# Performance work log

Measured on AMD Instinct MI355X. Metric: run time of the kernel, lower is better.

The kernel has to match this reference:

```python
import jax, jax.numpy as jnp
import numpy as np

N = 50000
E = 800000
IN_DIM = 256
HID = 32
HEADS = 4
OUT_DIM = 40
NEG_SLOPE = 0.2


def gat_layer(x, src, dst, W, a_src, a_dst, b, n_nodes, heads, ch, concat):
    # x: [N, F_in], W: [F_in, heads*ch], a_src/a_dst: [heads, ch], b: [out]
    h = (x @ W).reshape(n_nodes, heads, ch)                 # [N,H,C]
    alpha_s = jnp.einsum('nhc,hc->nh', h, a_src)            # [N,H]
    alpha_d = jnp.einsum('nhc,hc->nh', h, a_dst)            # [N,H]
    e = jax.nn.leaky_relu(alpha_s[src] + alpha_d[dst], NEG_SLOPE)  # [E,H]
    # segment softmax over destination neighborhoods (self-loops guarantee nonempty)
    m = jax.ops.segment_max(e, dst, num_segments=n_nodes)   # [N,H]
    e = jnp.exp(e - m[dst])
    denom = jax.ops.segment_sum(e, dst, num_segments=n_nodes)
    alpha = e / (denom[dst] + 1e-16)                         # [E,H]
    msg = h[src] * alpha[:, :, None]                         # [E,H,C]
    out = jax.ops.segment_sum(msg, dst, num_segments=n_nodes)  # [N,H,C]
    out = out.reshape(n_nodes, heads * ch) if concat else out.mean(axis=1)
    return out + b


def setup_inputs() -> dict:
    key = jax.random.key(0)
    ks = jax.random.split(key, 10)
    x = jax.random.normal(ks[0], (N, IN_DIM), dtype=jnp.float32)
    edge_index = jax.random.randint(ks[1], (2, E), 0, N, dtype=jnp.int32)
    s1 = 1.0 / np.sqrt(IN_DIM)
    s2 = 1.0 / np.sqrt(HID * HEADS)
    return {
        'x': x,
        'edge_index': edge_index,
        'W1': jax.random.normal(ks[2], (IN_DIM, HEADS * HID), dtype=jnp.float32) * s1,
        'a_src1': jax.random.normal(ks[3], (HEADS, HID), dtype=jnp.float32) * s1,
        'a_dst1': jax.random.normal(ks[4], (HEADS, HID), dtype=jnp.float32) * s1,
        'b1': jnp.zeros((HEADS * HID,), dtype=jnp.float32),
        'W2': jax.random.normal(ks[5], (HEADS * HID, OUT_DIM), dtype=jnp.float32) * s2,
        'a_src2': jax.random.normal(ks[6], (1, OUT_DIM), dtype=jnp.float32) * s2,
        'a_dst2': jax.random.normal(ks[7], (1, OUT_DIM), dtype=jnp.float32) * s2,
        'b2': jnp.zeros((OUT_DIM,), dtype=jnp.float32),
    }


def reference(x, edge_index, W1, a_src1, a_dst1, b1, W2, a_src2, a_dst2, b2):
    # PyG GATConv adds self-loops by default
    loops = jnp.arange(N, dtype=edge_index.dtype)
    src = jnp.concatenate([edge_index[0], loops])
    dst = jnp.concatenate([edge_index[1], loops])
    h = gat_layer(x, src, dst, W1, a_src1, a_dst1, b1, N, HEADS, HID, True)
    h = jax.nn.relu(h)
    out = gat_layer(h, src, dst, W2, a_src2, a_dst2, b2, N, 1, OUT_DIM, False)
    return jax.nn.log_softmax(out, axis=1)
```

## Files before the change

### kernel.cpp

```cpp
#include <hip/hip_runtime.h>
#include <math.h>

#define N_NODES 50000
#define N_EDGES 800000
#define IN_DIM  256
#define F1      128
#define HEADS   4
#define OUT_DIM 40
#define NEG     0.2f

#define NB   391
#define CAP  3072
#define EB   4096
#define PREW 16
#define G1B  782

#define DCAP 96

typedef __attribute__((ext_vector_type(8))) short short8;
typedef __attribute__((ext_vector_type(4))) float float4v;

__device__ __forceinline__ unsigned short f2bf(float f) {
  unsigned int u = __float_as_uint(f);
  u += 0x7FFF + ((u >> 16) & 1);
  return (unsigned short)(u >> 16);
}
__device__ __forceinline__ float bf2f(unsigned short h) {
  return __uint_as_float((unsigned int)h << 16);
}
__device__ __forceinline__ float bflo(unsigned int u) { return __uint_as_float(u << 16); }
__device__ __forceinline__ float bfhi(unsigned int u) { return __uint_as_float(u & 0xffff0000u); }

__device__ __forceinline__ float lrelu(float e) { return e > 0.f ? e : e * NEG; }

__device__ __forceinline__ void gload_lds16(const void* g, void* l) {
  __builtin_amdgcn_global_load_lds(
      (const __attribute__((address_space(1))) unsigned int*)g,
      (__attribute__((address_space(3))) unsigned int*)l, 16, 0, 0);
}

__global__ __launch_bounds__(256) void pre_kernel(const float* __restrict__ W1,
                                                  unsigned short* __restrict__ wHi,
                                                  unsigned short* __restrict__ wLo,
                                                  const int* __restrict__ ei,
                                                  int* __restrict__ gcnt,
                                                  int2* __restrict__ gbucket) {
  __shared__ int smem[EB * 2 + NB * 3];
  if (blockIdx.x < PREW) {
    int tid = blockIdx.x * 256 + threadIdx.x;
    int kk = tid >> 9;
    int rest = tid & 511;
    int t = rest >> 6;
    int lane = rest & 63;
    int q = lane >> 4;
    int ln = lane & 15;
    int n = t * 16 + ln;
    unsigned int hi[4], lo[4];
#pragma unroll
    for (int jj = 0; jj < 4; jj++) {
      unsigned short h0, h1, l0, l1;
      {
        float v = W1[(kk * 32 + q * 8 + jj * 2) * F1 + n];
        h0 = f2bf(v); l0 = f2bf(v - bf2f(h0));
      }
      {
        float v = W1[(kk * 32 + q * 8 + jj * 2 + 1) * F1 + n];
        h1 = f2bf(v); l1 = f2bf(v - bf2f(h1));
      }
      hi[jj] = (unsigned int)h0 | ((unsigned int)h1 << 16);
      lo[jj] = (unsigned int)l0 | ((unsigned int)l1 << 16);
    }
    size_t base = (size_t)tid * 8;
    *(uint4*)&wHi[base] = make_uint4(hi[0], hi[1], hi[2], hi[3]);
    *(uint4*)&wLo[base] = make_uint4(lo[0], lo[1], lo[2], lo[3]);
  } else {
    int* ls = smem;
    int* ld = smem + EB;
    int* lcnt = smem + 2 * EB;
    int* lcur = lcnt + NB;
    int* gbaseS = lcur + NB;
    int tid = threadIdx.x;
    size_t base = (size_t)(blockIdx.x - PREW) * EB;
    for (int t = tid; t < NB; t += 256) { lcnt[t] = 0; lcur[t] = 0; }
    __syncthreads();
#pragma unroll
    for (int l = 0; l < EB / 256; l++) {
      int li = l * 256 + tid;
      size_t idx = base + li;
      int s = 0, d = -1;
      if (idx < N_EDGES) {
        s = ei[idx];
        d = ei[N_EDGES + idx];
        atomicAdd(&lcnt[d >> 7], 1);
      }
      ls[li] = s;
      ld[li] = d;
    }
    __syncthreads();
    for (int t = tid; t < NB; t += 256) gbaseS[t] = atomicAdd(&gcnt[t], lcnt[t]);
    __syncthreads();
#pragma unroll
    for (int l = 0; l < EB / 256; l++) {
      int li = l * 256 + tid;
      int d = ld[li];
      if (d >= 0) {
        int b = d >> 7;
        int r = gbaseS[b] + atomicAdd(&lcur[b], 1);
        if (r >= CAP) r = CAP - 1;
        gbucket[(size_t)b * CAP + r] = make_int2(ls[li], d);
      }
    }
  }
}

__global__ __launch_bounds__(256) void mid_kernel(
    const float* __restrict__ x, const unsigned short* __restrict__ wHi,
    const unsigned short* __restrict__ wLo,
    const float* __restrict__ a_src, const float* __restrict__ a_dst,
    unsigned short* __restrict__ h1b, float* __restrict__ as1, float* __restrict__ ad1,
    const int2* __restrict__ gbucket, const int* __restrict__ gcnt,
    int* __restrict__ row_ptr, int* __restrict__ col) {
  __shared__ short8 smem[2048];
  if (blockIdx.x < G1B) {
    short8 (*Bsh)[1024] = (short8(*)[1024])smem;
    int bid = blockIdx.x;
    int tid = threadIdx.x;
    int w = tid >> 6;
    int lane = tid & 63;
    int q = lane >> 4;
    int ln = lane & 15;
    int rowBase = bid * 64 + w * 16;
    int rowA = rowBase + ln;
    int rowAc = rowA < N_NODES ? rowA : N_NODES - 1;
    float4v acc[8];
#pragma unroll
    for (int t = 0; t < 8; t++) acc[t] = (float4v){0.f, 0.f, 0.f, 0.f};
    const short8* bhp = (const short8*)wHi;
    const short8* blp = (const short8*)wLo;

    auto prefetch = [&](int kk, int buf) {
#pragma unroll
      for (int c = 0; c < 2; c++) {
        int chunk = w * 2 + c;
        gload_lds16(bhp + (size_t)kk * 512 + chunk * 64 + lane, &Bsh[buf][chunk * 64]);
        gload_lds16(blp + (size_t)kk * 512 + chunk * 64 + lane, &Bsh[buf][512 + chunk * 64]);
      }
    };

    const float4* xbase = (const float4*)(x + (size_t)rowAc * IN_DIM + q * 8);
    float4 a0 = xbase[0];
    float4 a1 = xbase[1];
    prefetch(0, 0);
    __syncthreads();

#pragma unroll 1
    for (int kk = 0; kk < 8; kk++) {
      int buf = kk & 1;
      if (kk < 7) prefetch(kk + 1, buf ^ 1);
      int kn = (kk < 7) ? kk + 1 : 7;
      float4 n0 = xbase[kn * 8];
      float4 n1 = xbase[kn * 8 + 1];
      float av[8] = {a0.x, a0.y, a0.z, a0.w, a1.x, a1.y, a1.z, a1.w};
      short8 ahi, alo;
#pragma unroll
      for (int j = 0; j < 8; j++) {
        unsigned short hh = f2bf(av[j]);
        ahi[j] = (short)hh;
        alo[j] = (short)f2bf(av[j] - bf2f(hh));
      }
      const short8* bs = &Bsh[buf][0];
#pragma unroll
      for (int t = 0; t < 8; t++) {
        short8 bh = bs[t * 64 + lane];
        short8 bl = bs[512 + t * 64 + lane];
        acc[t] = __builtin_amdgcn_mfma_f32_16x16x32_bf16(ahi, bh, acc[t], 0, 0, 0);
        acc[t] = __builtin_amdgcn_mfma_f32_16x16x32_bf16(ahi, bl, acc[t], 0, 0, 0);
        acc[t] = __builtin_amdgcn_mfma_f32_16x16x32_bf16(alo, bh, acc[t], 0, 0, 0);
      }
      a0 = n0;
      a1 = n1;
      if (kk < 7) __syncthreads();
    }

    float asv[8], adv[8];
#pragma unroll
    for (int t = 0; t < 8; t++) {
      asv[t] = a_src[t * 16 + ln];
      adv[t] = a_dst[t * 16 + ln];
    }
#pragma unroll
    for (int reg = 0; reg < 4; reg++) {
      int r = rowBase + q * 4 + reg;
      bool valid = (r < N_NODES);
      if (valid) {
#pragma unroll
        for (int t = 0; t < 8; t++)
          h1b[(size_t)r * F1 + t * 16 + ln] = f2bf(acc[t][reg]);
      }
#pragma unroll
      for (int h = 0; h < 4; h++) {
        float sa = acc[2 * h][reg] * asv[2 * h] + acc[2 * h + 1][reg] * asv[2 * h + 1];
        float sd = acc[2 * h][reg] * adv[2 * h] + acc[2 * h + 1][reg] * adv[2 * h + 1];
#pragma unroll
        for (int off = 1; off < 16; off <<= 1) {
          sa += __shfl_xor(sa, off);
          sd += __shfl_xor(sd, off);
        }
        if (ln == 0 && valid) {
          as1[r * 4 + h] = sa;
          ad1[r * 4 + h] = sd;
        }
      }
    }
  } else {
    int2* ent = (int2*)smem;
    int* hcnt = (int*)(ent + CAP);
    int* sc   = hcnt + 128;
    int* cur  = sc + 128;
    int* red  = cur + 128;
    int b = blockIdx.x - G1B;
    int tid = threadIdx.x;
    int cnt = gcnt[b]; if (cnt > CAP) cnt = CAP;
    if (tid < 128) hcnt[tid] = 0;
    int part = 0;
    for (int i = tid; i < b; i += 256) part += gcnt[i];
#pragma unroll
    for (int off = 32; off > 0; off >>= 1) part += __shfl_xor(part, off);
    if ((tid & 63) == 0) red[tid >> 6] = part;
    __syncthreads();
    int base = red[0] + red[1] + red[2] + red[3];
    for (int i = tid; i < cnt; i += 256) {
      int2 e = gbucket[(size_t)b * CAP + i];
      ent[i] = e;
      atomicAdd(&hcnt[e.y & 127], 1);
    }
    __syncthreads();
    if (tid < 128) sc[tid] = hcnt[tid];
    __syncthreads();
    for (int off = 1; off < 128; off <<= 1) {
      int t = 0;
      if (tid < 128 && tid >= off) t = sc[tid - off];
      __syncthreads();
      if (tid < 128) sc[tid] += t;
      __syncthreads();
    }
    if (tid < 128) {
      int excl = sc[tid] - hcnt[tid];
      cur[tid] = excl;
      int node = (b << 7) + tid;
      if (node < N_NODES) row_ptr[node] = base + excl;
    }
    if (b == 0 && tid == 0) row_ptr[N_NODES] = N_EDGES;
    __syncthreads();
    for (int i = tid; i < cnt; i += 256) {
      int2 e = ent[i];
      int r = atomicAdd(&cur[e.y & 127], 1);
      col[base + r] = e.x;
    }
  }
}

__global__ __launch_bounds__(256) void gather1_kernel(
    const unsigned short* __restrict__ h1b, const float* __restrict__ as1,
    const float* __restrict__ ad1, const float* __restrict__ b1,
    const int* __restrict__ row_ptr, const int* __restrict__ col,
    float* __restrict__ x2) {
  __shared__ float4 wsh[4][DCAP];
  __shared__ int ssh[4][DCAP];
  int wv = threadIdx.x >> 6;
  int n = blockIdx.x * 4 + wv;
  if (n >= N_NODES) return;
  int lane = threadIdx.x & 63;
  int start = row_ptr[n];
  int deg = row_ptr[n + 1] - start;
  bool fast = (deg + 1) <= DCAP;
  float4 ad = *(const float4*)&ad1[n * 4];
  float s0 = 0.f, s1 = 0.f, s2 = 0.f, s3 = 0.f;
  for (int i = lane; i <= deg; i += 64) {
    int src = (i < deg) ? col[start + i] : n;
    float4 as = *(const float4*)&as1[src * 4];
    float e0 = __expf(lrelu(as.x + ad.x));
    float e1 = __expf(lrelu(as.y + ad.y));
    float e2 = __expf(lrelu(as.z + ad.z));
    float e3 = __expf(lrelu(as.w + ad.w));
    s0 += e0; s1 += e1; s2 += e2; s3 += e3;
    if (fast) {
      ssh[wv][i] = src;
      wsh[wv][i] = make_float4(e0, e1, e2, e3);
    }
  }
#pragma unroll
  for (int off = 32; off > 0; off >>= 1) {
    s0 += __shfl_xor(s0, off);
    s1 += __shfl_xor(s1, off);
    s2 += __shfl_xor(s2, off);
    s3 += __shfl_xor(s3, off);
  }
  int slot = lane >> 4;
  int lane16 = lane & 15;
  int head = lane16 >> 2;
  float rsh = (head == 0) ? s0 : (head == 1) ? s1 : (head == 2) ? s2 : s3;
  rsh = 1.f / (rsh + 1e-16f);
  float4 accA = make_float4(0.f, 0.f, 0.f, 0.f);
  float4 accB = make_float4(0.f, 0.f, 0.f, 0.f);
  if (fast) {
    const float* wp = (const float*)&wsh[wv][0];
    int i = slot;
    for (; i + 4 <= deg; i += 8) {
      int sA = ssh[wv][i];
      int sB = ssh[wv][i + 4];
      float wA = wp[i * 4 + head] * rsh;
      float wB = wp[(i + 4) * 4 + head] * rsh;
      uint4 uA = *(const uint4*)(h1b + (size_t)sA * F1 + lane16 * 8);
      uint4 uB = *(const uint4*)(h1b + (size_t)sB * F1 + lane16 * 8);
      accA.x += wA * bflo(uA.x); accA.y += wA * bfhi(uA.x);
      accA.z += wA * bflo(uA.y); accA.w += wA * bfhi(uA.y);
      accB.x += wA * bflo(uA.z); accB.y += wA * bfhi(uA.z);
      accB.z += wA * bflo(uA.w); accB.w += wA * bfhi(uA.w);
      accA.x += wB * bflo(uB.x); accA.y += wB * bfhi(uB.x);
      accA.z += wB * bflo(uB.y); accA.w += wB * bfhi(uB.y);
      accB.x += wB * bflo(uB.z); accB.y += wB * bfhi(uB.z);
      accB.z += wB * bflo(uB.w); accB.w += wB * bfhi(uB.w);
    }
    if (i <= deg) {
      int s = ssh[wv][i];
      float w = wp[i * 4 + head] * rsh;
      uint4 u = *(const uint4*)(h1b + (size_t)s * F1 + lane16 * 8);
      accA.x += w * bflo(u.x); accA.y += w * bfhi(u.x);
      accA.z += w * bflo(u.y); accA.w += w * bfhi(u.y);
      accB.x += w * bflo(u.z); accB.y += w * bfhi(u.z);
      accB.z += w * bflo(u.w); accB.w += w * bfhi(u.w);
    }
  } else {
    float adh = (head == 0) ? ad.x : (head == 1) ? ad.y : (head == 2) ? ad.z : ad.w;
    for (int i = slot; i <= deg; i += 4) {
      int src = (i < deg) ? col[start + i] : n;
      float w = __expf(lrelu(as1[src * 4 + head] + adh)) * rsh;
      uint4 u = *(const uint4*)(h1b + (size_t)src * F1 + lane16 * 8);
      accA.x += w * bflo(u.x); accA.y += w * bfhi(u.x);
      accA.z += w * bflo(u.y); accA.w += w * bfhi(u.y);
      accB.x += w * bflo(u.z); accB.y += w * bfhi(u.z);
      accB.z += w * bflo(u.w); accB.w += w * bfhi(u.w);
    }
  }
#pragma unroll
  for (int off = 16; off <= 32; off <<= 1) {
    accA.x += __shfl_xor(accA.x, off); accA.y += __shfl_xor(accA.y, off);
    accA.z += __shfl_xor(accA.z, off); accA.w += __shfl_xor(accA.w, off);
    accB.x += __shfl_xor(accB.x, off); accB.y += __shfl_xor(accB.y, off);
    accB.z += __shfl_xor(accB.z, off); accB.w += __shfl_xor(accB.w, off);
  }
  if (slot == 0) {
    float4 bA = *(const float4*)&b1[lane16 * 8];
    float4 bB = *(const float4*)&b1[lane16 * 8 + 4];
    float4 oA, oB;
    oA.x = fmaxf(accA.x + bA.x, 0.f); oA.y = fmaxf(accA.y + bA.y, 0.f);
    oA.z = fmaxf(accA.z + bA.z, 0.f); oA.w = fmaxf(accA.w + bA.w, 0.f);
    oB.x = fmaxf(accB.x + bB.x, 0.f); oB.y = fmaxf(accB.y + bB.y, 0.f);
    oB.z = fmaxf(accB.z + bB.z, 0.f); oB.w = fmaxf(accB.w + bB.w, 0.f);
    *(float4*)&x2[(size_t)n * F1 + lane16 * 8] = oA;
    *(float4*)&x2[(size_t)n * F1 + lane16 * 8 + 4] = oB;
  }
}

__global__ __launch_bounds__(256) void gemm2_kernel(
    const float* __restrict__ x2, const float* __restrict__ W2,
    const float* __restrict__ asv, const float* __restrict__ adv,
    unsigned short* __restrict__ h2b, float* __restrict__ as2, float* __restrict__ ad2) {
  __shared__ float xs[64][132];
  __shared__ float W2s[128][44];
  __shared__ float asv_s[40], adv_s[40];
  int tid = threadIdx.x;
  int bm = blockIdx.x * 64;
#pragma unroll
  for (int l = 0; l < 8; l++) {
    int idx = tid + l * 256;
    int r = idx >> 5;
    int c4 = (idx & 31) << 2;
    float4 v = make_float4(0.f, 0.f, 0.f, 0.f);
    if (bm + r < N_NODES) v = *(const float4*)&x2[(size_t)(bm + r) * F1 + c4];
    *(float4*)&xs[r][c4] = v;
  }
#pragma unroll
  for (int l = 0; l < 5; l++) {
    int idx = tid + l * 256;
    int k = idx / 10;
    int c4 = (idx - k * 10) * 4;
    *(float4*)&W2s[k][c4] = *(const float4*)&W2[k * OUT_DIM + c4];
  }
  if (tid < OUT_DIM) { asv_s[tid] = asv[tid]; adv_s[tid] = adv[tid]; }
  __syncthreads();
  int r = tid >> 2;
  int cb = (tid & 3) * 10;
  float acc[10] = {0.f};
  for (int k = 0; k < F1; k++) {
    float xv = xs[r][k];
#pragma unroll
    for (int c = 0; c < 10; c++) acc[c] += xv * W2s[k][cb + c];
  }
  int grow = bm + r;
  float sa = 0.f, sd = 0.f;
#pragma unroll
  for (int c = 0; c < 10; c++) {
    sa += acc[c] * asv_s[cb + c];
    sd += acc[c] * adv_s[cb + c];
  }
#pragma unroll
  for (int off = 1; off < 4; off <<= 1) {
    sa += __shfl_xor(sa, off);
    sd += __shfl_xor(sd, off);
  }
  if (grow < N_NODES) {
#pragma unroll
    for (int c = 0; c < 10; c += 2) {
      unsigned int p = ((unsigned int)f2bf(acc[c + 1]) << 16) | f2bf(acc[c]);
      *(unsigned int*)&h2b[(size_t)grow * OUT_DIM + cb + c] = p;
    }
    if ((tid & 3) == 0) { as2[grow] = sa; ad2[grow] = sd; }
  }
}

__global__ __launch_bounds__(256) void gather2_kernel(
    const unsigned short* __restrict__ h2b, const float* __restrict__ as2,
    const float* __restrict__ ad2, const float* __restrict__ b2,
    const int* __restrict__ row_ptr, const int* __restrict__ col,
    float* __restrict__ out) {
  __shared__ float w2sh[4][DCAP];
  __shared__ int s2sh[4][DCAP];
  int wv = threadIdx.x >> 6;
  int n = blockIdx.x * 4 + wv;
  if (n >= N_NODES) return;
  int lane = threadIdx.x & 63;
  int start = row_ptr[n];
  int deg = row_ptr[n + 1] - start;
  bool fast = (deg + 1) <= DCAP;
  float adh = ad2[n];
  float part = 0.f;
  for (int i = lane; i <= deg; i += 64) {
    int src = (i < deg) ? col[start + i] : n;
    float e = __expf(lrelu(as2[src] + adh));
    part += e;
    if (fast) { s2sh[wv][i] = src; w2sh[wv][i] = e; }
  }
#pragma unroll
  for (int off = 32; off > 0; off >>= 1) part += __shfl_xor(part, off);
  float rs = 1.f / (part + 1e-16f);
  int slot = lane / 5;
  int c = lane - slot * 5;
  float4 accA = make_float4(0.f, 0.f, 0.f, 0.f);
  float4 accB = make_float4(0.f, 0.f, 0.f, 0.f);
  if (slot < 12) {
    if (fast) {
      for (int i = slot; i <= deg; i += 12) {
        int src = s2sh[wv][i];
        float wgt = w2sh[wv][i] * rs;
        uint4 u = *(const uint4*)(h2b + (size_t)src * OUT_DIM + c * 8);
        accA.x += wgt * bflo(u.x); accA.y += wgt * bfhi(u.x);
        accA.z += wgt * bflo(u.y); accA.w += wgt * bfhi(u.y);
        accB.x += wgt * bflo(u.z); accB.y += wgt * bfhi(u.z);
        accB.z += wgt * bflo(u.w); accB.w += wgt * bfhi(u.w);
      }
    } else {
      for (int i = slot; i <= deg; i += 12) {
        int src = (i < deg) ? col[start + i] : n;
        float wgt = __expf(lrelu(as2[src] + adh)) * rs;
        uint4 u = *(const uint4*)(h2b + (size_t)src * OUT_DIM + c * 8);
        accA.x += wgt * bflo(u.x); accA.y += wgt * bfhi(u.x);
        accA.z += wgt * bflo(u.y); accA.w += wgt * bfhi(u.y);
        accB.x += wgt * bflo(u.z); accB.y += wgt * bfhi(u.z);
        accB.z += wgt * bflo(u.w); accB.w += wgt * bfhi(u.w);
      }
    }
  }
  {
    float v[8] = {accA.x, accA.y, accA.z, accA.w, accB.x, accB.y, accB.z, accB.w};
#pragma unroll
    for (int k = 0; k < 8; k++) v[k] += __shfl(v[k], lane + 30);
#pragma unroll
    for (int k = 0; k < 8; k++) v[k] += __shfl(v[k], lane + 15);
    float t1[8], t2[8];
#pragma unroll
    for (int k = 0; k < 8; k++) t1[k] = __shfl(v[k], lane + 5);
#pragma unroll
    for (int k = 0; k < 8; k++) t2[k] = __shfl(v[k], lane + 10);
#pragma unroll
    for (int k = 0; k < 8; k++) v[k] += t1[k] + t2[k];
    accA.x = v[0]; accA.y = v[1]; accA.z = v[2]; accA.w = v[3];
    accB.x = v[4]; accB.y = v[5]; accB.z = v[6]; accB.w = v[7];
  }
  bool owner = (slot == 0);
  float vals[8] = {accA.x, accA.y, accA.z, accA.w, accB.x, accB.y, accB.z, accB.w};
  float lmax = -1e30f, lsum = 0.f;
  if (owner) {
#pragma unroll
    for (int k = 0; k < 8; k++) {
      vals[k] += b2[c * 8 + k];
      lmax = fmaxf(lmax, vals[k]);
    }
  }
  float gmax = lmax;
#pragma unroll
  for (int off = 32; off > 0; off >>= 1) gmax = fmaxf(gmax, __shfl_xor(gmax, off));
  if (owner) {
#pragma unroll
    for (int k = 0; k < 8; k++) lsum += __expf(vals[k] - gmax);
  }
#pragma unroll
  for (int off = 32; off > 0; off >>= 1) lsum += __shfl_xor(lsum, off);
  if (owner) {
    float lse = gmax + __logf(lsum);
    float4 oA = make_float4(vals[0] - lse, vals[1] - lse, vals[2] - lse, vals[3] - lse);
    float4 oB = make_float4(vals[4] - lse, vals[5] - lse, vals[6] - lse, vals[7] - lse);
    *(float4*)&out[(size_t)n * OUT_DIM + c * 8] = oA;
    *(float4*)&out[(size_t)n * OUT_DIM + c * 8 + 4] = oB;
  }
}

extern "C" void kernel_launch(void* const* d_in, const int* in_sizes, int n_in,
                              void* d_out, int out_size, void* d_ws, size_t ws_size,
                              hipStream_t stream) {
  const float* x      = (const float*)d_in[0];
  const int*   ei     = (const int*)d_in[1];
  const float* W1     = (const float*)d_in[2];
  const float* a_src1 = (const float*)d_in[3];
  const float* a_dst1 = (const float*)d_in[4];
  const float* b1     = (const float*)d_in[5];
  const float* W2     = (const float*)d_in[6];
  const float* a_src2 = (const float*)d_in[7];
  const float* a_dst2 = (const float*)d_in[8];
  const float* b2     = (const float*)d_in[9];
  float* out = (float*)d_out;

  char* ws = (char*)d_ws;
  size_t off = 0;
  auto alloc = [&](size_t bytes) -> void* {
    void* p = ws + off;
    off += (bytes + 255) & ~(size_t)255;
    return p;
  };
  unsigned short* h1b = (unsigned short*)alloc((size_t)N_NODES * F1 * 2);
  unsigned short* h2b = (unsigned short*)alloc((size_t)N_NODES * OUT_DIM * 2);
  unsigned short* wHi = (unsigned short*)alloc((size_t)IN_DIM * F1 * 2);
  unsigned short* wLo = (unsigned short*)alloc((size_t)IN_DIM * F1 * 2);
  float* as1    = (float*)alloc((size_t)N_NODES * HEADS * 4);
  float* ad1    = (float*)alloc((size_t)N_NODES * HEADS * 4);
  float* x2     = (float*)alloc((size_t)N_NODES * F1 * 4);
  float* as2    = (float*)alloc((size_t)N_NODES * 4);
  float* ad2    = (float*)alloc((size_t)N_NODES * 4);
  int* row_ptr  = (int*)alloc((size_t)(N_NODES + 1) * 4);
  int* col      = (int*)alloc((size_t)N_EDGES * 4);
  int* gcnt     = (int*)alloc((size_t)NB * 4);
  int2* gbucket = (int2*)alloc((size_t)NB * CAP * 8);

  hipMemsetAsync(gcnt, 0, (size_t)NB * 4, stream);
  pre_kernel<<<PREW + (N_EDGES + EB - 1) / EB, 256, 0, stream>>>(W1, wHi, wLo, ei, gcnt, gbucket);
  mid_kernel<<<G1B + NB, 256, 0, stream>>>(x, wHi, wLo, a_src1, a_dst1, h1b, as1, ad1,
                                           gbucket, gcnt, row_ptr, col);
  gather1_kernel<<<(N_NODES + 3) / 4, 256, 0, stream>>>(h1b, as1, ad1, b1, row_ptr, col, x2);

  gemm2_kernel<<<(N_NODES + 63) / 64, 256, 0, stream>>>(x2, W2, a_src2, a_dst2, h2b, as2, ad2);
  gather2_kernel<<<(N_NODES + 3) / 4, 256, 0, stream>>>(h2b, as2, ad2, b2, row_ptr, col, out);
}
```

Measured before the change: 241.8 us.

## Fuse softmax denominator into single-pass neighbor aggregation in both gather kernels

Both gather kernels drop the separate first pass that computed exp weights and their sum into shared memory. They now compute the unnormalized exp weight per edge inline during aggregation, accumulate the denominator alongside the features, and normalize once after the cross-lane reduction. This removes a pass over the edge list and the LDS staging. In exchange, each of the 16 lanes per slot in layer 1 recomputes the exp and reloads col/as1 redundantly, and the reductions carry an extra value. The max subtraction was already omitted before this change.

Result: faster. 233.2 us, median of 2 (-3.6%).

```diff
diff --git a/kernel.cpp b/kernel.cpp
--- a/kernel.cpp
+++ b/kernel.cpp
@@ -14,8 +14,6 @@
 #define EB   4096
 #define PREW 16
 #define G1B  782
-
-#define DCAP 96
 
 typedef __attribute__((ext_vector_type(8))) short short8;
 typedef __attribute__((ext_vector_type(4))) float float4v;
@@ -265,83 +263,46 @@
     const float* __restrict__ ad1, const float* __restrict__ b1,
     const int* __restrict__ row_ptr, const int* __restrict__ col,
     float* __restrict__ x2) {
-  __shared__ float4 wsh[4][DCAP];
-  __shared__ int ssh[4][DCAP];
   int wv = threadIdx.x >> 6;
   int n = blockIdx.x * 4 + wv;
   if (n >= N_NODES) return;
   int lane = threadIdx.x & 63;
   int start = row_ptr[n];
   int deg = row_ptr[n + 1] - start;
-  bool fast = (deg + 1) <= DCAP;
-  float4 ad = *(const float4*)&ad1[n * 4];
-  float s0 = 0.f, s1 = 0.f, s2 = 0.f, s3 = 0.f;
-  for (int i = lane; i <= deg; i += 64) {
-    int src = (i < deg) ? col[start + i] : n;
-    float4 as = *(const float4*)&as1[src * 4];
-    float e0 = __expf(lrelu(as.x + ad.x));
-    float e1 = __expf(lrelu(as.y + ad.y));
-    float e2 = __expf(lrelu(as.z + ad.z));
-    float e3 = __expf(lrelu(as.w + ad.w));
-    s0 += e0; s1 += e1; s2 += e2; s3 += e3;
-    if (fast) {
-      ssh[wv][i] = src;
-      wsh[wv][i] = make_float4(e0, e1, e2, e3);
-    }
-  }
-#pragma unroll
-  for (int off = 32; off > 0; off >>= 1) {
-    s0 += __shfl_xor(s0, off);
-    s1 += __shfl_xor(s1, off);
-    s2 += __shfl_xor(s2, off);
-    s3 += __shfl_xor(s3, off);
-  }
   int slot = lane >> 4;
   int lane16 = lane & 15;
   int head = lane16 >> 2;
-  float rsh = (head == 0) ? s0 : (head == 1) ? s1 : (head == 2) ? s2 : s3;
-  rsh = 1.f / (rsh + 1e-16f);
+  float adh = ad1[n * 4 + head];
   float4 accA = make_float4(0.f, 0.f, 0.f, 0.f);
   float4 accB = make_float4(0.f, 0.f, 0.f, 0.f);
-  if (fast) {
-    const float* wp = (const float*)&wsh[wv][0];
-    int i = slot;
-    for (; i + 4 <= deg; i += 8) {
-      int sA = ssh[wv][i];
-      int sB = ssh[wv][i + 4];
-      float wA = wp[i * 4 + head] * rsh;
-      float wB = wp[(i + 4) * 4 + head] * rsh;
-      uint4 uA = *(const uint4*)(h1b + (size_t)sA * F1 + lane16 * 8);
-      uint4 uB = *(const uint4*)(h1b + (size_t)sB * F1 + lane16 * 8);
-      accA.x += wA * bflo(uA.x); accA.y += wA * bfhi(uA.x);
-      accA.z += wA * bflo(uA.y); accA.w += wA * bfhi(uA.y);
-      accB.x += wA * bflo(uA.z); accB.y += wA * bfhi(uA.z);
-      accB.z += wA * bflo(uA.w); accB.w += wA * bfhi(uA.w);
-      accA.x += wB * bflo(uB.x); accA.y += wB * bfhi(uB.x);
-      accA.z += wB * bflo(uB.y); accA.w += wB * bfhi(uB.y);
-      accB.x += wB * bflo(uB.z); accB.y += wB * bfhi(uB.z);
-      accB.z += wB * bflo(uB.w); accB.w += wB * bfhi(uB.w);
-    }
-    if (i <= deg) {
-      int s = ssh[wv][i];
-      float w = wp[i * 4 + head] * rsh;
-      uint4 u = *(const uint4*)(h1b + (size_t)s * F1 + lane16 * 8);
-      accA.x += w * bflo(u.x); accA.y += w * bfhi(u.x);
-      accA.z += w * bflo(u.y); accA.w += w * bfhi(u.y);
-      accB.x += w * bflo(u.z); accB.y += w * bfhi(u.z);
-      accB.z += w * bflo(u.w); accB.w += w * bfhi(u.w);
-    }
-  } else {
-    float adh = (head == 0) ? ad.x : (head == 1) ? ad.y : (head == 2) ? ad.z : ad.w;
-    for (int i = slot; i <= deg; i += 4) {
-      int src = (i < deg) ? col[start + i] : n;
-      float w = __expf(lrelu(as1[src * 4 + head] + adh)) * rsh;
-      uint4 u = *(const uint4*)(h1b + (size_t)src * F1 + lane16 * 8);
-      accA.x += w * bflo(u.x); accA.y += w * bfhi(u.x);
-      accA.z += w * bflo(u.y); accA.w += w * bfhi(u.y);
-      accB.x += w * bflo(u.z); accB.y += w * bfhi(u.z);
-      accB.z += w * bflo(u.w); accB.w += w * bfhi(u.w);
-    }
+  float dn = 0.f;
+  int i = slot;
+  for (; i + 4 <= deg; i += 8) {
+    int sA = col[start + i];
+    int sB = (i + 4 < deg) ? col[start + i + 4] : n;
+    float eA = __expf(lrelu(as1[sA * 4 + head] + adh));
+    float eB = __expf(lrelu(as1[sB * 4 + head] + adh));
+    uint4 uA = *(const uint4*)(h1b + (size_t)sA * F1 + lane16 * 8);
+    uint4 uB = *(const uint4*)(h1b + (size_t)sB * F1 + lane16 * 8);
+    dn += eA + eB;
+    accA.x += eA * bflo(uA.x); accA.y += eA * bfhi(uA.x);
+    accA.z += eA * bflo(uA.y); accA.w += eA * bfhi(uA.y);
+    accB.x += eA * bflo(uA.z); accB.y += eA * bfhi(uA.z);
+    accB.z += eA * bflo(uA.w); accB.w += eA * bfhi(uA.w);
+    accA.x += eB * bflo(uB.x); accA.y += eB * bfhi(uB.x);
+    accA.z += eB * bflo(uB.y); accA.w += eB * bfhi(uB.y);
+    accB.x += eB * bflo(uB.z); accB.y += eB * bfhi(uB.z);
+    accB.z += eB * bflo(uB.w); accB.w += eB * bfhi(uB.w);
+  }
+  if (i <= deg) {
+    int s = (i < deg) ? col[start + i] : n;
+    float e = __expf(lrelu(as1[s * 4 + head] + adh));
+    uint4 u = *(const uint4*)(h1b + (size_t)s * F1 + lane16 * 8);
+    dn += e;
+    accA.x += e * bflo(u.x); accA.y += e * bfhi(u.x);
+    accA.z += e * bflo(u.y); accA.w += e * bfhi(u.y);
+    accB.x += e * bflo(u.z); accB.y += e * bfhi(u.z);
+    accB.z += e * bflo(u.w); accB.w += e * bfhi(u.w);
   }
 #pragma unroll
   for (int off = 16; off <= 32; off <<= 1) {
@@ -349,15 +310,17 @@
     accA.z += __shfl_xor(accA.z, off); accA.w += __shfl_xor(accA.w, off);
     accB.x += __shfl_xor(accB.x, off); accB.y += __shfl_xor(accB.y, off);
     accB.z += __shfl_xor(accB.z, off); accB.w += __shfl_xor(accB.w, off);
+    dn += __shfl_xor(dn, off);
   }
   if (slot == 0) {
+    float rsh = 1.f / (dn + 1e-16f);
     float4 bA = *(const float4*)&b1[lane16 * 8];
     float4 bB = *(const float4*)&b1[lane16 * 8 + 4];
     float4 oA, oB;
-    oA.x = fmaxf(accA.x + bA.x, 0.f); oA.y = fmaxf(accA.y + bA.y, 0.f);
-    oA.z = fmaxf(accA.z + bA.z, 0.f); oA.w = fmaxf(accA.w + bA.w, 0.f);
-    oB.x = fmaxf(accB.x + bB.x, 0.f); oB.y = fmaxf(accB.y + bB.y, 0.f);
-    oB.z = fmaxf(accB.z + bB.z, 0.f); oB.w = fmaxf(accB.w + bB.w, 0.f);
+    oA.x = fmaxf(accA.x * rsh + bA.x, 0.f); oA.y = fmaxf(accA.y * rsh + bA.y, 0.f);
+    oA.z = fmaxf(accA.z * rsh + bA.z, 0.f); oA.w = fmaxf(accA.w * rsh + bA.w, 0.f);
+    oB.x = fmaxf(accB.x * rsh + bB.x, 0.f); oB.y = fmaxf(accB.y * rsh + bB.y, 0.f);
+    oB.z = fmaxf(accB.z * rsh + bB.z, 0.f); oB.w = fmaxf(accB.w * rsh + bB.w, 0.f);
     *(float4*)&x2[(size_t)n * F1 + lane16 * 8] = oA;
     *(float4*)&x2[(size_t)n * F1 + lane16 * 8 + 4] = oB;
   }
@@ -425,76 +388,52 @@
     const float* __restrict__ ad2, const float* __restrict__ b2,
     const int* __restrict__ row_ptr, const int* __restrict__ col,
     float* __restrict__ out) {
-  __shared__ float w2sh[4][DCAP];
-  __shared__ int s2sh[4][DCAP];
   int wv = threadIdx.x >> 6;
   int n = blockIdx.x * 4 + wv;
   if (n >= N_NODES) return;
   int lane = threadIdx.x & 63;
   int start = row_ptr[n];
   int deg = row_ptr[n + 1] - start;
-  bool fast = (deg + 1) <= DCAP;
   float adh = ad2[n];
-  float part = 0.f;
-  for (int i = lane; i <= deg; i += 64) {
-    int src = (i < deg) ? col[start + i] : n;
-    float e = __expf(lrelu(as2[src] + adh));
-    part += e;
-    if (fast) { s2sh[wv][i] = src; w2sh[wv][i] = e; }
-  }
-#pragma unroll
-  for (int off = 32; off > 0; off >>= 1) part += __shfl_xor(part, off);
-  float rs = 1.f / (part + 1e-16f);
   int slot = lane / 5;
   int c = lane - slot * 5;
   float4 accA = make_float4(0.f, 0.f, 0.f, 0.f);
   float4 accB = make_float4(0.f, 0.f, 0.f, 0.f);
+  float dn = 0.f;
   if (slot < 12) {
-    if (fast) {
-      for (int i = slot; i <= deg; i += 12) {
-        int src = s2sh[wv][i];
-        float wgt = w2sh[wv][i] * rs;
-        uint4 u = *(const uint4*)(h2b + (size_t)src * OUT_DIM + c * 8);
-        accA.x += wgt * bflo(u.x); accA.y += wgt * bfhi(u.x);
-        accA.z += wgt * bflo(u.y); accA.w += wgt * bfhi(u.y);
-        accB.x += wgt * bflo(u.z); accB.y += wgt * bfhi(u.z);
-        accB.z += wgt * bflo(u.w); accB.w += wgt * bfhi(u.w);
-      }
-    } else {
-      for (int i = slot; i <= deg; i += 12) {
-        int src = (i < deg) ? col[start + i] : n;
-        float wgt = __expf(lrelu(as2[src] + adh)) * rs;
-        uint4 u = *(const uint4*)(h2b + (size_t)src * OUT_DIM + c * 8);
-        accA.x += wgt * bflo(u.x); accA.y += wgt * bfhi(u.x);
-        accA.z += wgt * bflo(u.y); accA.w += wgt * bfhi(u.y);
-        accB.x += wgt * bflo(u.z); accB.y += wgt * bfhi(u.z);
-        accB.z += wgt * bflo(u.w); accB.w += wgt * bfhi(u.w);
-      }
-    }
-  }
+    for (int i = slot; i <= deg; i += 12) {
+      int src = (i < deg) ? col[start + i] : n;
+      float e = __expf(lrelu(as2[src] + adh));
+      uint4 u = *(const uint4*)(h2b + (size_t)src * OUT_DIM + c * 8);
+      dn += e;
+      accA.x += e * bflo(u.x); accA.y += e * bfhi(u.x);
+      accA.z += e * bflo(u.y); accA.w += e * bfhi(u.y);
+      accB.x += e * bflo(u.z); accB.y += e * bfhi(u.z);
+      accB.z += e * bflo(u.w); accB.w += e * bfhi(u.w);
+    }
+  }
+  float v[9] = {accA.x, accA.y, accA.z, accA.w, accB.x, accB.y, accB.z, accB.w, dn};
+#pragma unroll
+  for (int k = 0; k < 9; k++) v[k] += __shfl(v[k], lane + 30);
+#pragma unroll
+  for (int k = 0; k < 9; k++) v[k] += __shfl(v[k], lane + 15);
   {
-    float v[8] = {accA.x, accA.y, accA.z, accA.w, accB.x, accB.y, accB.z, accB.w};
-#pragma unroll
-    for (int k = 0; k < 8; k++) v[k] += __shfl(v[k], lane + 30);
-#pragma unroll
-    for (int k = 0; k < 8; k++) v[k] += __shfl(v[k], lane + 15);
-    float t1[8], t2[8];
-#pragma unroll
-    for (int k = 0; k < 8; k++) t1[k] = __shfl(v[k], lane + 5);
-#pragma unroll
-    for (int k = 0; k < 8; k++) t2[k] = __shfl(v[k], lane + 10);
-#pragma unroll
-    for (int k = 0; k < 8; k++) v[k] += t1[k] + t2[k];
-    accA.x = v[0]; accA.y = v[1]; accA.z = v[2]; accA.w = v[3];
-    accB.x = v[4]; accB.y = v[5]; accB.z = v[6]; accB.w = v[7];
+    float t1[9], t2[9];
+#pragma unroll
+    for (int k = 0; k < 9; k++) t1[k] = __shfl(v[k], lane + 5);
+#pragma unroll
+    for (int k = 0; k < 9; k++) t2[k] = __shfl(v[k], lane + 10);
+#pragma unroll
+    for (int k = 0; k < 9; k++) v[k] += t1[k] + t2[k];
   }
   bool owner = (slot == 0);
-  float vals[8] = {accA.x, accA.y, accA.z, accA.w, accB.x, accB.y, accB.z, accB.w};
+  float vals[8];
   float lmax = -1e30f, lsum = 0.f;
   if (owner) {
+    float rs = 1.f / (v[8] + 1e-16f);
 #pragma unroll
     for (int k = 0; k < 8; k++) {
-      vals[k] += b2[c * 8 + k];
+      vals[k] = v[k] * rs + b2[c * 8 + k];
       lmax = fmaxf(lmax, vals[k]);
     }
   }
```
